# Kernel tuning notes

Hardware: AMD Instinct MI355X
Metric: run time of the kernel (lower is better)

## Reference

```python
import jax, jax.numpy as jnp
import numpy as np


def setup_inputs() -> dict:
    key = jax.random.key(0)
    k1, k2 = jax.random.split(key)
    x = jax.random.normal(k1, (16, 256, 4096), dtype=jnp.float32)          # [B, D, T]
    codebooks = jax.random.normal(k2, (8, 1024, 256), dtype=jnp.float32)   # [n_q, bins, D]
    return {"x": x, "codebooks": codebooks}


def _quantize_one(residual, embed):
    """residual: [B, T, D]; embed: [bins, D] -> (quantize [B,T,D], idx [B,T])."""
    # negative squared euclidean distance (encodec euclidean codebook)
    x_sq = jnp.sum(residual * residual, axis=-1, keepdims=True)            # [B, T, 1]
    e_sq = jnp.sum(embed * embed, axis=-1)                                  # [bins]
    dots = jnp.einsum("btd,nd->btn", residual, embed)                       # [B, T, bins]
    dist = -(x_sq - 2.0 * dots + e_sq)                                      # [B, T, bins]
    idx = jnp.argmax(dist, axis=-1)                                         # [B, T] int
    quantize = embed[idx]                                                   # gather [B, T, D]
    return quantize, idx


def reference(x, codebooks):
    """Residual VQ forward (inference path, EMA updates omitted).
    x: [B, D, T]; codebooks: [n_q, bins, D].
    Returns (quantized [B, D, T], codes [n_q, B, T]).
    """
    n_q = codebooks.shape[0]
    residual = jnp.transpose(x, (0, 2, 1))                                  # [B, T, D]
    quantized_out = jnp.zeros_like(residual)
    codes = []
    for q in range(n_q):  # small fixed structural loop over quantizer stages
        quantize, idx = _quantize_one(residual, codebooks[q])
        # straight-through estimator as in encodec VectorQuantization
        quantize = residual + jax.lax.stop_gradient(quantize - residual)
        residual = residual - quantize
        quantized_out = quantized_out + quantize
        codes.append(idx)
    quantized = jnp.transpose(quantized_out, (0, 2, 1))                     # [B, D, T]
    codes = jnp.stack(codes, axis=0)                                        # [n_q, B, T]
    return quantized, codes
```

## Files before the change

### kernel.cpp

```cpp
#include <hip/hip_runtime.h>


#define BB   16
#define DD   256
#define TT   4096
#define NQ   8
#define BINS 1024
#define DELTA 4.0f
#define SOFF  8192.0f
#define OUTQ ((size_t)BB * DD * TT)

typedef _Float16 half8 __attribute__((ext_vector_type(8)));
typedef float    facc  __attribute__((ext_vector_type(4)));

#define MFMA16(A, B, C) __builtin_amdgcn_mfma_f32_16x16x32_f16((A), (B), (C), 0, 0, 0)

__global__ __launch_bounds__(256)
void rvq_pack_h16(const float* __restrict__ cb, _Float16* __restrict__ pks) {
    int gid = blockIdx.x * 256 + threadIdx.x;
    int s   = gid & 7;
    int bin = (gid >> 3) & 1023;
    int q   = gid >> 13;
    const float* src = cb + ((size_t)(q * BINS + bin)) * DD + s * 32;
    int cc    = q * 32 + (bin >> 5);
    int nf    = (bin >> 4) & 1;
    int c     = bin & 15;
    int plane = nf * 8 + s;
    size_t base = (size_t)cc * 8192 + (size_t)plane * 512 + c * 8;
    #pragma unroll
    for (int g = 0; g < 4; ++g) {
        float4 v0 = *(const float4*)(src + g * 8);
        float4 v1 = *(const float4*)(src + g * 8 + 4);
        float vv[8] = { v0.x, v0.y, v0.z, v0.w, v1.x, v1.y, v1.z, v1.w };
        half8 h8;
        #pragma unroll
        for (int j = 0; j < 8; ++j) h8[j] = (_Float16)vv[j];
        *(half8*)&pks[base + g * 128] = h8;
    }
}

__global__ __launch_bounds__(256)
void rvq_esq_off(const float* __restrict__ cb, float* __restrict__ hoff) {
    int q = blockIdx.x;
    const float* e = cb + (size_t)q * BINS * DD;
    for (int bin = threadIdx.x; bin < BINS; bin += 256) {
        const float4* row = (const float4*)(e + (size_t)bin * DD);
        float s = 0.f;
        #pragma unroll 8
        for (int i = 0; i < DD / 4; ++i) {
            float4 v = row[i];
            s += v.x * v.x + v.y * v.y + v.z * v.z + v.w * v.w;
        }
        hoff[q * BINS + bin] = SOFF - 8.0f * s;
    }
}

__global__ __launch_bounds__(256, 2)
void rvq_mfma7_kernel(const float* __restrict__ x, const float* __restrict__ cb,
                      const _Float16* __restrict__ pks, const float* __restrict__ hoff,
                      float* __restrict__ out)
{
    __shared__ alignas(16) _Float16 btile[2][2][16][512];
    __shared__ float esq_lds[BINS];
    __shared__ unsigned short best_lds[4][32];
    __shared__ unsigned short hist_lds[4][NQ][32];

    const int tid = threadIdx.x;
    const int w   = tid >> 6;
    const int l   = tid & 63;
    const int c   = l & 15;
    const int g   = l >> 4;

    const int blk = blockIdx.x;
    const int b   = blk >> 5;
    const int t0  = (blk & 31) * 128;
    const int tw  = t0 + w * 32;

    const char* gsrc0 = (const char*)pks + w * 8192 + (l << 4);

    auto issue_pair = [&](int p, int bu) {
        p &= 127;
        const char* src = gsrc0 + (size_t)p * 32768;
        char* dst = (char*)(&btile[bu][0][0][0]) + w * 8192;
        #pragma unroll
        for (int i = 0; i < 8; ++i) {
            __builtin_amdgcn_global_load_lds(
                (const __attribute__((address_space(1))) unsigned int*)(src + i * 1024),
                (__attribute__((address_space(3))) unsigned int*)(dst + i * 1024),
                16, 0, 0);
        }
    };

    issue_pair(0, 0);

    half8 rh[2][8], rl[2][8];
    {
        const float* xb = x + (size_t)b * DD * TT;
        #pragma unroll
        for (int s = 0; s < 8; ++s) {
            #pragma unroll
            for (int j = 0; j < 8; ++j) {
                int d = s * 32 + g * 8 + j;
                #pragma unroll
                for (int m = 0; m < 2; ++m) {
                    int t = tw + m * 16 + c;
                    float v = 16.0f * xb[(size_t)d * TT + t];
                    _Float16 h = (_Float16)v;
                    rh[m][s][j] = h;
                    rl[m][s][j] = (_Float16)(v - (float)h);
                }
            }
        }
    }
    {
        float4 v = *(const float4*)(hoff + tid * 4);
        *(float4*)&esq_lds[tid * 4] = v;
    }
    __syncthreads();

    float p1[2][4], p2[2][4], p3[2][4];

    auto reset_slots = [&]() {
        #pragma unroll
        for (int m = 0; m < 2; ++m)
            #pragma unroll
            for (int j = 0; j < 4; ++j) { p1[m][j] = 0.f; p2[m][j] = 0.f; p3[m][j] = 0.f; }
    };

    auto compute_chunk = [&](int bu, int pc, int ch) {
        facc a00 = {0.f,0.f,0.f,0.f}, a01 = {0.f,0.f,0.f,0.f};
        facc a10 = {0.f,0.f,0.f,0.f}, a11 = {0.f,0.f,0.f,0.f};
        const int roff = g * 128 + c * 8;
        const float q0 = esq_lds[ch * 32 + c];
        const float q1 = esq_lds[ch * 32 + 16 + c];
        const _Float16 (*bt)[512] = btile[bu][pc];

        __builtin_amdgcn_s_setprio(1);
        #pragma unroll
        for (int s = 0; s < 8; ++s) {
            half8 b0 = *(const half8*)&bt[s][roff];
            half8 b1 = *(const half8*)&bt[8 + s][roff];
            a00 = MFMA16(rh[0][s], b0, a00);
            a10 = MFMA16(rh[1][s], b0, a10);
            a01 = MFMA16(rh[0][s], b1, a01);
            a11 = MFMA16(rh[1][s], b1, a11);
        }
        __builtin_amdgcn_s_setprio(0);

        const unsigned idx0 = 1023u - (unsigned)(ch * 32 + c);
        const unsigned idx1 = idx0 - 16u;
        #pragma unroll
        for (int fm = 0; fm < 2; ++fm) {
            #pragma unroll
            for (int fj = 0; fj < 4; ++fj) {
                float s0 = (fm ? a10[fj] : a00[fj]) + q0;
                float s1 = (fm ? a11[fj] : a01[fj]) + q1;
                float v0 = __builtin_bit_cast(float,
                             (__builtin_bit_cast(unsigned, s0) & ~1023u) | idx0);
                float v1 = __builtin_bit_cast(float,
                             (__builtin_bit_cast(unsigned, s1) & ~1023u) | idx1);
                float h1 = fmaxf(p1[fm][fj], v0), l1 = fminf(p1[fm][fj], v0);
                float h2 = fmaxf(p2[fm][fj], l1), l2 = fminf(p2[fm][fj], l1);
                p1[fm][fj] = h1; p2[fm][fj] = h2; p3[fm][fj] = fmaxf(p3[fm][fj], l2);
                h1 = fmaxf(p1[fm][fj], v1); l1 = fminf(p1[fm][fj], v1);
                h2 = fmaxf(p2[fm][fj], l1); l2 = fminf(p2[fm][fj], l1);
                p1[fm][fj] = h1; p2[fm][fj] = h2; p3[fm][fj] = fmaxf(p3[fm][fj], l2);
            }
        }
    };

    auto refine3 = [&](int tkl, int qq, int c1, int c2, int c3) -> int {
        int t = tw + tkl;
        double pa = 0.0, pb = 0.0, pc = 0.0;
        const float* e1p = cb + (size_t)(qq * BINS + c1) * DD;
        const float* e2p = cb + (size_t)(qq * BINS + c2) * DD;
        const float* e3p = cb + (size_t)(qq * BINS + c3) * DD;
        #pragma unroll
        for (int dd = 0; dd < 4; ++dd) {
            int d = l * 4 + dd;
            float rv = x[((size_t)b * DD + d) * TT + t];
            for (int k = 0; k < qq; ++k) {
                int hb = hist_lds[w][k][tkl];
                rv -= cb[(size_t)(k * BINS + hb) * DD + d];
            }
            float e1v = e1p[d], e2v = e2p[d], e3v = e3p[d];
            pa += (double)e1v * (2.0 * (double)rv - (double)e1v);
            pb += (double)e2v * (2.0 * (double)rv - (double)e2v);
            pc += (double)e3v * (2.0 * (double)rv - (double)e3v);
        }
        #pragma unroll
        for (int mk = 1; mk < 64; mk <<= 1) {
            pa += __shfl_xor(pa, mk);
            pb += __shfl_xor(pb, mk);
            pc += __shfl_xor(pc, mk);
        }
        int wbin = c1; double pw = pa;
        if (pb > pw || (pb == pw && c2 < wbin)) { pw = pb; wbin = c2; }
        if (pc > pw || (pc == pw && c3 < wbin)) { pw = pc; wbin = c3; }
        return wbin;
    };

    auto stage_end = [&](int qq) {
        int  bch[2][4], cn2[2][4], cn3[2][4];
        bool gate[2][4];
        #pragma unroll
        for (int fm = 0; fm < 2; ++fm) {
            #pragma unroll
            for (int fj = 0; fj < 4; ++fj) {
                float a1 = p1[fm][fj], a2 = p2[fm][fj], a3 = p3[fm][fj];
                #pragma unroll
                for (int mk = 1; mk < 16; mk <<= 1) {
                    float b1 = __shfl_xor(a1, mk);
                    float b2 = __shfl_xor(a2, mk);
                    float b3 = __shfl_xor(a3, mk);
                    float lo1 = fminf(a1, b1);
                    float m22 = fmaxf(a2, b2);
                    float r1  = fmaxf(a1, b1);
                    float r2  = fmaxf(lo1, m22);
                    float r3  = fmaxf(fminf(lo1, m22), fmaxf(fminf(a2, b2), fmaxf(a3, b3)));
                    a1 = r1; a2 = r2; a3 = r3;
                }
                bch[fm][fj] = 1023 - (int)(__builtin_bit_cast(unsigned, a1) & 1023u);
                cn2[fm][fj] = 1023 - (int)(__builtin_bit_cast(unsigned, a2) & 1023u);
                cn3[fm][fj] = 1023 - (int)(__builtin_bit_cast(unsigned, a3) & 1023u);
                gate[fm][fj] = (a1 - a2 <= DELTA);
            }
        }
        bool anyg = gate[0][0] | gate[0][1] | gate[0][2] | gate[0][3]
                  | gate[1][0] | gate[1][1] | gate[1][2] | gate[1][3];
        if (__any(anyg)) {
            #pragma unroll
            for (int fm = 0; fm < 2; ++fm) {
                #pragma unroll
                for (int fj = 0; fj < 4; ++fj) {
                    unsigned long long nm = __ballot(gate[fm][fj]);
                    if (nm) {
                        for (int g2 = 0; g2 < 4; ++g2) {
                            if ((nm >> (g2 * 16)) & 1ull) {
                                int c1 = __shfl(bch[fm][fj], g2 * 16);
                                int c2 = __shfl(cn2[fm][fj], g2 * 16);
                                int c3 = __shfl(cn3[fm][fj], g2 * 16);
                                int tkl = fm * 16 + g2 * 4 + fj;
                                int wb = refine3(tkl, qq, c1, c2, c3);
                                if (g == g2) bch[fm][fj] = wb;
                            }
                        }
                    }
                }
            }
        }

        if (c == 0) {
            #pragma unroll
            for (int fm = 0; fm < 2; ++fm)
                #pragma unroll
                for (int fj = 0; fj < 4; ++fj) {
                    int tkl = fm * 16 + g * 4 + fj;
                    best_lds[w][tkl] = (unsigned short)bch[fm][fj];
                    hist_lds[w][qq][tkl] = (unsigned short)bch[fm][fj];
                    out[OUTQ + ((size_t)qq * BB + b) * TT + tw + tkl] = (float)bch[fm][fj];
                }
        }

        #pragma unroll
        for (int m = 0; m < 2; ++m) {
            int bin = best_lds[w][m * 16 + c];
            const float* ep = cb + (size_t)(qq * BINS + bin) * DD + g * 8;
            #pragma unroll
            for (int s = 0; s < 8; ++s) {
                float4 e0 = *(const float4*)(ep + s * 32);
                float4 e1 = *(const float4*)(ep + s * 32 + 4);
                float ev[8] = { e0.x, e0.y, e0.z, e0.w, e1.x, e1.y, e1.z, e1.w };
                #pragma unroll
                for (int j = 0; j < 8; ++j) {
                    float rv = (float)rh[m][s][j] + (float)rl[m][s][j];
                    float nr = rv - 16.0f * ev[j];
                    _Float16 nh = (_Float16)nr;
                    rh[m][s][j] = nh;
                    rl[m][s][j] = (_Float16)(nr - (float)nh);
                }
            }
        }
    };

    int buf = 0;
    #pragma unroll 1
    for (int q = 0; q < NQ; ++q) {
        reset_slots();
        #pragma unroll 1
        for (int p = 0; p < 16; ++p) {
            issue_pair(q * 16 + p + 1, buf ^ 1);
            compute_chunk(buf, 0, 2 * p);
            compute_chunk(buf, 1, 2 * p + 1);
            if (p == 15) stage_end(q);
            __syncthreads();
            buf ^= 1;
        }
        if (q + 1 < NQ) {
            float4 v = *(const float4*)(hoff + (q + 1) * BINS + tid * 4);
            *(float4*)&esq_lds[tid * 4] = v;
            __syncthreads();
        }
    }

    {
        const float* xb = x + (size_t)b * DD * TT;
        float* ob = out + (size_t)b * DD * TT;
        #pragma unroll
        for (int s = 0; s < 8; ++s)
            #pragma unroll
            for (int j = 0; j < 8; ++j) {
                int d = s * 32 + g * 8 + j;
                #pragma unroll
                for (int m = 0; m < 2; ++m) {
                    int t = tw + m * 16 + c;
                    float rv = ((float)rh[m][s][j] + (float)rl[m][s][j]) * 0.0625f;
                    ob[(size_t)d * TT + t] = xb[(size_t)d * TT + t] - rv;
                }
            }
    }
}

#define TOK_PER_BLK 32
#define BIN_CHUNK   128
#define KC          32
#define EPAD        36
#define RPAD        260
#define FDELTA      0.0078125f

#define FUPD2(S, BIN, B1, I1, B2, I2)                                        \
    if ((S) > (B2) || ((S) == (B2) && (BIN) < (I2))) {                      \
        if ((S) > (B1) || ((S) == (B1) && (BIN) < (I1))) {                  \
            B2 = B1; I2 = I1; B1 = (S); I1 = (BIN);                         \
        } else { B2 = (S); I2 = (BIN); }                                    \
    }

__global__ __launch_bounds__(256, 2)
void rvq_esq_kernel(const float* __restrict__ cb, float* __restrict__ esq) {
    int q = blockIdx.x;
    const float* e = cb + (size_t)q * BINS * DD;
    for (int bin = threadIdx.x; bin < BINS; bin += 256) {
        const float4* row = (const float4*)(e + (size_t)bin * DD);
        float s = 0.f;
        #pragma unroll 8
        for (int i = 0; i < DD / 4; ++i) {
            float4 v = row[i];
            s += v.x * v.x + v.y * v.y + v.z * v.z + v.w * v.w;
        }
        esq[q * BINS + bin] = s;
    }
}

__global__ __launch_bounds__(256, 2)
void rvq_main_kernel(const float* __restrict__ x, const float* __restrict__ cb,
                     const float* __restrict__ esq, float* __restrict__ out) {
    __shared__ float r_lds[TOK_PER_BLK][RPAD];
    __shared__ float e_lds[BIN_CHUNK][EPAD];
    __shared__ float red_s[16][2][TOK_PER_BLK];
    __shared__ int   red_i[16][2][TOK_PER_BLK];
    __shared__ int   best_lds2[TOK_PER_BLK];

    const int tid = threadIdx.x;
    const int blk = blockIdx.x;
    const int b   = blk >> 7;
    const int t0  = (blk & 127) * TOK_PER_BLK;

    {
        const int tl = tid & 31;
        const int d0 = (tid >> 5) * 32;
        const float* xp = x + (size_t)b * DD * TT + t0 + tl;
        for (int dd = 0; dd < 32; ++dd) {
            int d = d0 + dd;
            r_lds[tl][d] = xp[(size_t)d * TT];
        }
    }
    __syncthreads();

    const int ty = tid >> 4;
    const int tx = tid & 15;

    for (int q = 0; q < NQ; ++q) {
        const float* eb = cb + (size_t)q * BINS * DD;
        const float* es = esq + q * BINS;
        float b1[2] = {-1e30f, -1e30f}, b2[2] = {-1e30f, -1e30f};
        int   i1[2] = {0x7fffffff, 0x7fffffff}, i2[2] = {0x7fffffff, 0x7fffffff};

        for (int cch = 0; cch < BINS / BIN_CHUNK; ++cch) {
            float acc[2][8];
            #pragma unroll
            for (int i = 0; i < 2; ++i)
                #pragma unroll
                for (int j = 0; j < 8; ++j) acc[i][j] = 0.f;

            for (int kc = 0; kc < DD / KC; ++kc) {
                __syncthreads();
                {
                    const int col  = tid & 7;
                    const int row0 = tid >> 3;
                    const float* src = eb + (size_t)(cch * BIN_CHUNK) * DD + kc * KC;
                    #pragma unroll
                    for (int rr = 0; rr < 4; ++rr) {
                        int row = row0 + rr * 32;
                        float4 v = *(const float4*)(src + (size_t)row * DD + col * 4);
                        *(float4*)&e_lds[row][col * 4] = v;
                    }
                }
                __syncthreads();
                #pragma unroll
                for (int k4 = 0; k4 < KC / 4; ++k4) {
                    float4 r0 = *(const float4*)&r_lds[tx][kc * KC + k4 * 4];
                    float4 r1 = *(const float4*)&r_lds[tx + 16][kc * KC + k4 * 4];
                    #pragma unroll
                    for (int bi = 0; bi < 8; ++bi) {
                        float4 e4 = *(const float4*)&e_lds[ty + 16 * bi][k4 * 4];
                        acc[0][bi] += r0.x * e4.x + r0.y * e4.y + r0.z * e4.z + r0.w * e4.w;
                        acc[1][bi] += r1.x * e4.x + r1.y * e4.y + r1.z * e4.z + r1.w * e4.w;
                    }
                }
            }
            #pragma unroll
            for (int bi = 0; bi < 8; ++bi) {
                int bin = cch * BIN_CHUNK + ty + 16 * bi;
                float half_esq = 0.5f * es[bin];
                float s0 = acc[0][bi] - half_esq;
                float s1v = acc[1][bi] - half_esq;
                FUPD2(s0, bin, b1[0], i1[0], b2[0], i2[0]);
                FUPD2(s1v, bin, b1[1], i1[1], b2[1], i2[1]);
            }
        }

        #pragma unroll
        for (int k = 0; k < 2; ++k) {
            red_s[ty][k][tx]      = k ? b2[0] : b1[0];
            red_i[ty][k][tx]      = k ? i2[0] : i1[0];
            red_s[ty][k][tx + 16] = k ? b2[1] : b1[1];
            red_i[ty][k][tx + 16] = k ? i2[1] : i1[1];
        }
        __syncthreads();

        if (tid < TOK_PER_BLK) {
            float g1 = -1e30f, g2 = -1e30f; int gi1 = 0x7fffffff, gi2 = 0x7fffffff;
            #pragma unroll
            for (int j = 0; j < 16; ++j) {
                #pragma unroll
                for (int k = 0; k < 2; ++k) {
                    float s = red_s[j][k][tid]; int ii = red_i[j][k][tid];
                    FUPD2(s, ii, g1, gi1, g2, gi2);
                }
            }
            int bif;
            if (g1 - g2 <= FDELTA) {
                const float* rrow = r_lds[tid];
                double sc[2]; int id2[2] = { gi1, gi2 };
                for (int cc2 = 0; cc2 < 2; ++cc2) {
                    const float* ep = eb + (size_t)id2[cc2] * DD;
                    double acc2 = 0.0;
                    #pragma unroll 4
                    for (int d = 0; d < DD; ++d) {
                        double ev = (double)ep[d];
                        acc2 += ev * (2.0 * (double)rrow[d] - ev);
                    }
                    sc[cc2] = acc2;
                }
                bif = (sc[0] > sc[1] || (sc[0] == sc[1] && id2[0] < id2[1])) ? id2[0] : id2[1];
            } else {
                bif = gi1;
            }
            best_lds2[tid] = bif;
            out[OUTQ + (size_t)q * (BB * TT) + (size_t)b * TT + t0 + tid] = (float)bif;
        }
        __syncthreads();

        {
            const int tok  = tid >> 3;
            const int part = tid & 7;
            const int bin  = best_lds2[tok];
            const float* ep = eb + (size_t)bin * DD + part * 32;
            float* rp = &r_lds[tok][part * 32];
            #pragma unroll
            for (int dd = 0; dd < 32; ++dd) rp[dd] -= ep[dd];
        }
        __syncthreads();
    }

    {
        const int tl = tid & 31;
        const int d0 = (tid >> 5) * 32;
        const float* xp = x + (size_t)b * DD * TT + t0 + tl;
        float*       op = out + (size_t)b * DD * TT + t0 + tl;
        for (int dd = 0; dd < 32; ++dd) {
            int d = d0 + dd;
            op[(size_t)d * TT] = xp[(size_t)d * TT] - r_lds[tl][d];
        }
    }
}

extern "C" void kernel_launch(void* const* d_in, const int* in_sizes, int n_in,
                              void* d_out, int out_size, void* d_ws, size_t ws_size,
                              hipStream_t stream) {
    const float* x  = (const float*)d_in[0];
    const float* cb = (const float*)d_in[1];
    float* out = (float*)d_out;

    const size_t PKS_BYTES = (size_t)NQ * BINS * DD * 2;
    const size_t NEED = PKS_BYTES + (size_t)NQ * BINS * 4;

    if (ws_size >= NEED) {
        _Float16* pks = (_Float16*)d_ws;
        float* hoff = (float*)((char*)d_ws + PKS_BYTES);
        rvq_pack_h16<<<(NQ * BINS * 8) / 256, 256, 0, stream>>>(cb, pks);
        rvq_esq_off<<<NQ, 256, 0, stream>>>(cb, hoff);
        rvq_mfma7_kernel<<<512, 256, 0, stream>>>(x, cb, pks, hoff, out);
    } else {
        float* esq = (float*)d_ws;
        rvq_esq_kernel<<<NQ, 256, 0, stream>>>(cb, esq);
        rvq_main_kernel<<<(BB * TT) / TOK_PER_BLK, 256, 0, stream>>>(x, cb, esq, out);
    }
}
```

Baseline: 627.2 us.

## Triple-buffer codebook chunks with fine-grained vmcnt waits and med3 top-3 update

```diff
diff --git a/kernel.cpp b/kernel.cpp
--- a/kernel.cpp
+++ b/kernel.cpp
@@ -56,11 +56,11 @@
 }
 
 __global__ __launch_bounds__(256, 2)
-void rvq_mfma7_kernel(const float* __restrict__ x, const float* __restrict__ cb,
-                      const _Float16* __restrict__ pks, const float* __restrict__ hoff,
-                      float* __restrict__ out)
+void rvq_mfma10_kernel(const float* __restrict__ x, const float* __restrict__ cb,
+                       const _Float16* __restrict__ pks, const float* __restrict__ hoff,
+                       float* __restrict__ out)
 {
-    __shared__ alignas(16) _Float16 btile[2][2][16][512];
+    __shared__ alignas(16) _Float16 btile[3][16][512];
     __shared__ float esq_lds[BINS];
     __shared__ unsigned short best_lds[4][32];
     __shared__ unsigned short hist_lds[4][NQ][32];
@@ -76,22 +76,19 @@
     const int t0  = (blk & 31) * 128;
     const int tw  = t0 + w * 32;
 
-    const char* gsrc0 = (const char*)pks + w * 8192 + (l << 4);
-
-    auto issue_pair = [&](int p, int bu) {
-        p &= 127;
-        const char* src = gsrc0 + (size_t)p * 32768;
-        char* dst = (char*)(&btile[bu][0][0][0]) + w * 8192;
-        #pragma unroll
-        for (int i = 0; i < 8; ++i) {
+    const char* gsrc0 = (const char*)pks + w * 4096 + (l << 4);
+
+    auto issue_chunk = [&](int k, int bu) {
+        const char* src = gsrc0 + (size_t)k * 16384;
+        char* dst = (char*)(&btile[bu][0][0]) + w * 4096;
+        #pragma unroll
+        for (int i = 0; i < 4; ++i) {
             __builtin_amdgcn_global_load_lds(
                 (const __attribute__((address_space(1))) unsigned int*)(src + i * 1024),
                 (__attribute__((address_space(3))) unsigned int*)(dst + i * 1024),
                 16, 0, 0);
         }
     };
-
-    issue_pair(0, 0);
 
     half8 rh[2][8], rl[2][8];
     {
@@ -127,13 +124,13 @@
             for (int j = 0; j < 4; ++j) { p1[m][j] = 0.f; p2[m][j] = 0.f; p3[m][j] = 0.f; }
     };
 
-    auto compute_chunk = [&](int bu, int pc, int ch) {
+    auto compute_chunk = [&](int bu, int ch) {
         facc a00 = {0.f,0.f,0.f,0.f}, a01 = {0.f,0.f,0.f,0.f};
         facc a10 = {0.f,0.f,0.f,0.f}, a11 = {0.f,0.f,0.f,0.f};
         const int roff = g * 128 + c * 8;
         const float q0 = esq_lds[ch * 32 + c];
         const float q1 = esq_lds[ch * 32 + 16 + c];
-        const _Float16 (*bt)[512] = btile[bu][pc];
+        const _Float16 (*bt)[512] = btile[bu];
 
         __builtin_amdgcn_s_setprio(1);
         #pragma unroll
@@ -159,12 +156,14 @@
                              (__builtin_bit_cast(unsigned, s0) & ~1023u) | idx0);
                 float v1 = __builtin_bit_cast(float,
                              (__builtin_bit_cast(unsigned, s1) & ~1023u) | idx1);
-                float h1 = fmaxf(p1[fm][fj], v0), l1 = fminf(p1[fm][fj], v0);
-                float h2 = fmaxf(p2[fm][fj], l1), l2 = fminf(p2[fm][fj], l1);
-                p1[fm][fj] = h1; p2[fm][fj] = h2; p3[fm][fj] = fmaxf(p3[fm][fj], l2);
-                h1 = fmaxf(p1[fm][fj], v1); l1 = fminf(p1[fm][fj], v1);
-                h2 = fmaxf(p2[fm][fj], l1); l2 = fminf(p2[fm][fj], l1);
-                p1[fm][fj] = h1; p2[fm][fj] = h2; p3[fm][fj] = fmaxf(p3[fm][fj], l2);
+                float o1 = p1[fm][fj], o2 = p2[fm][fj], o3 = p3[fm][fj];
+                p1[fm][fj] = fmaxf(o1, v0);
+                p2[fm][fj] = __builtin_amdgcn_fmed3f(v0, o1, o2);
+                p3[fm][fj] = __builtin_amdgcn_fmed3f(v0, o2, o3);
+                o1 = p1[fm][fj]; o2 = p2[fm][fj]; o3 = p3[fm][fj];
+                p1[fm][fj] = fmaxf(o1, v1);
+                p2[fm][fj] = __builtin_amdgcn_fmed3f(v1, o1, o2);
+                p3[fm][fj] = __builtin_amdgcn_fmed3f(v1, o2, o3);
             }
         }
     };
@@ -283,19 +282,27 @@
         }
     };
 
-    int buf = 0;
     #pragma unroll 1
     for (int q = 0; q < NQ; ++q) {
         reset_slots();
+        const int base = q * 32;
+        issue_chunk(base + 0, 0);
+        issue_chunk(base + 1, 1);
         #pragma unroll 1
-        for (int p = 0; p < 16; ++p) {
-            issue_pair(q * 16 + p + 1, buf ^ 1);
-            compute_chunk(buf, 0, 2 * p);
-            compute_chunk(buf, 1, 2 * p + 1);
-            if (p == 15) stage_end(q);
-            __syncthreads();
-            buf ^= 1;
-        }
+        for (int ch = 0; ch < 32; ++ch) {
+            __builtin_amdgcn_sched_barrier(0);
+            if (ch < 31) {
+                asm volatile("s_waitcnt vmcnt(4)" ::: "memory");
+            } else {
+                asm volatile("s_waitcnt vmcnt(0)" ::: "memory");
+            }
+            __builtin_amdgcn_s_barrier();
+            __builtin_amdgcn_sched_barrier(0);
+            if (ch + 2 < 32) issue_chunk(base + ch + 2, (ch + 2) % 3);
+            compute_chunk(ch % 3, ch);
+        }
+        stage_end(q);
+        __syncthreads();
         if (q + 1 < NQ) {
             float4 v = *(const float4*)(hoff + (q + 1) * BINS + tid * 4);
             *(float4*)&esq_lds[tid * 4] = v;
@@ -510,7 +517,7 @@
         float* hoff = (float*)((char*)d_ws + PKS_BYTES);
         rvq_pack_h16<<<(NQ * BINS * 8) / 256, 256, 0, stream>>>(cb, pks);
         rvq_esq_off<<<NQ, 256, 0, stream>>>(cb, hoff);
-        rvq_mfma7_kernel<<<512, 256, 0, stream>>>(x, cb, pks, hoff, out);
+        rvq_mfma10_kernel<<<512, 256, 0, stream>>>(x, cb, pks, hoff, out);
     } else {
         float* esq = (float*)d_ws;
         rvq_esq_kernel<<<NQ, 256, 0, stream>>>(cb, esq);
```

Measured after the change: 653.4 us. 4.2% more time.

## Load codebook fragments directly into registers instead of LDS double-buffering

Applied to the files above, without the earlier changes.

```diff
diff --git a/kernel.cpp b/kernel.cpp
--- a/kernel.cpp
+++ b/kernel.cpp
@@ -22,11 +22,9 @@
     int bin = (gid >> 3) & 1023;
     int q   = gid >> 13;
     const float* src = cb + ((size_t)(q * BINS + bin)) * DD + s * 32;
-    int cc    = q * 32 + (bin >> 5);
-    int nf    = (bin >> 4) & 1;
+    int cc    = q * 64 + (bin >> 4);
     int c     = bin & 15;
-    int plane = nf * 8 + s;
-    size_t base = (size_t)cc * 8192 + (size_t)plane * 512 + c * 8;
+    size_t base = (size_t)cc * 4096 + (size_t)s * 512 + c * 8;
     #pragma unroll
     for (int g = 0; g < 4; ++g) {
         float4 v0 = *(const float4*)(src + g * 8);
@@ -56,11 +54,10 @@
 }
 
 __global__ __launch_bounds__(256, 2)
-void rvq_mfma7_kernel(const float* __restrict__ x, const float* __restrict__ cb,
-                      const _Float16* __restrict__ pks, const float* __restrict__ hoff,
-                      float* __restrict__ out)
+void rvq_mfma11_kernel(const float* __restrict__ x, const float* __restrict__ cb,
+                       const _Float16* __restrict__ pks, const float* __restrict__ hoff,
+                       float* __restrict__ out)
 {
-    __shared__ alignas(16) _Float16 btile[2][2][16][512];
     __shared__ float esq_lds[BINS];
     __shared__ unsigned short best_lds[4][32];
     __shared__ unsigned short hist_lds[4][NQ][32];
@@ -76,22 +73,7 @@
     const int t0  = (blk & 31) * 128;
     const int tw  = t0 + w * 32;
 
-    const char* gsrc0 = (const char*)pks + w * 8192 + (l << 4);
-
-    auto issue_pair = [&](int p, int bu) {
-        p &= 127;
-        const char* src = gsrc0 + (size_t)p * 32768;
-        char* dst = (char*)(&btile[bu][0][0][0]) + w * 8192;
-        #pragma unroll
-        for (int i = 0; i < 8; ++i) {
-            __builtin_amdgcn_global_load_lds(
-                (const __attribute__((address_space(1))) unsigned int*)(src + i * 1024),
-                (__attribute__((address_space(3))) unsigned int*)(dst + i * 1024),
-                16, 0, 0);
-        }
-    };
-
-    issue_pair(0, 0);
+    const char* pkbase = (const char*)pks + ((l >> 4) * 256 + (l & 15) * 16);
 
     half8 rh[2][8], rl[2][8];
     {
@@ -120,54 +102,38 @@
 
     float p1[2][4], p2[2][4], p3[2][4];
 
-    auto reset_slots = [&]() {
-        #pragma unroll
-        for (int m = 0; m < 2; ++m)
-            #pragma unroll
-            for (int j = 0; j < 4; ++j) { p1[m][j] = 0.f; p2[m][j] = 0.f; p3[m][j] = 0.f; }
-    };
-
-    auto compute_chunk = [&](int bu, int pc, int ch) {
-        facc a00 = {0.f,0.f,0.f,0.f}, a01 = {0.f,0.f,0.f,0.f};
-        facc a10 = {0.f,0.f,0.f,0.f}, a11 = {0.f,0.f,0.f,0.f};
-        const int roff = g * 128 + c * 8;
-        const float q0 = esq_lds[ch * 32 + c];
-        const float q1 = esq_lds[ch * 32 + 16 + c];
-        const _Float16 (*bt)[512] = btile[bu][pc];
-
-        __builtin_amdgcn_s_setprio(1);
-        #pragma unroll
-        for (int s = 0; s < 8; ++s) {
-            half8 b0 = *(const half8*)&bt[s][roff];
-            half8 b1 = *(const half8*)&bt[8 + s][roff];
-            a00 = MFMA16(rh[0][s], b0, a00);
-            a10 = MFMA16(rh[1][s], b0, a10);
-            a01 = MFMA16(rh[0][s], b1, a01);
-            a11 = MFMA16(rh[1][s], b1, a11);
-        }
-        __builtin_amdgcn_s_setprio(0);
-
-        const unsigned idx0 = 1023u - (unsigned)(ch * 32 + c);
-        const unsigned idx1 = idx0 - 16u;
-        #pragma unroll
-        for (int fm = 0; fm < 2; ++fm) {
-            #pragma unroll
-            for (int fj = 0; fj < 4; ++fj) {
-                float s0 = (fm ? a10[fj] : a00[fj]) + q0;
-                float s1 = (fm ? a11[fj] : a01[fj]) + q1;
-                float v0 = __builtin_bit_cast(float,
-                             (__builtin_bit_cast(unsigned, s0) & ~1023u) | idx0);
-                float v1 = __builtin_bit_cast(float,
-                             (__builtin_bit_cast(unsigned, s1) & ~1023u) | idx1);
-                float h1 = fmaxf(p1[fm][fj], v0), l1 = fminf(p1[fm][fj], v0);
-                float h2 = fmaxf(p2[fm][fj], l1), l2 = fminf(p2[fm][fj], l1);
-                p1[fm][fj] = h1; p2[fm][fj] = h2; p3[fm][fj] = fmaxf(p3[fm][fj], l2);
-                h1 = fmaxf(p1[fm][fj], v1); l1 = fminf(p1[fm][fj], v1);
-                h2 = fmaxf(p2[fm][fj], l1); l2 = fminf(p2[fm][fj], l1);
-                p1[fm][fj] = h1; p2[fm][fj] = h2; p3[fm][fj] = fmaxf(p3[fm][fj], l2);
-            }
-        }
-    };
+    half8 Bx[8], By[8];
+
+#define LOADB(BSET, K) do {                                                  \
+    const char* _src = pkbase + (size_t)(K) * 8192;                          \
+    _Pragma("unroll")                                                        \
+    for (int _s = 0; _s < 8; ++_s)                                           \
+        BSET[_s] = *(const half8*)(_src + _s * 1024);                        \
+} while (0)
+
+#define COMPUTE(BSET, CH) do {                                               \
+    facc _a0 = {0.f,0.f,0.f,0.f}, _a1 = {0.f,0.f,0.f,0.f};                   \
+    _Pragma("unroll")                                                        \
+    for (int _s = 0; _s < 8; ++_s) {                                         \
+        _a0 = MFMA16(rh[0][_s], BSET[_s], _a0);                              \
+        _a1 = MFMA16(rh[1][_s], BSET[_s], _a1);                              \
+    }                                                                        \
+    const float _q0 = esq_lds[(CH) * 16 + c];                                \
+    const unsigned _idx0 = 1023u - (unsigned)((CH) * 16 + c);                \
+    _Pragma("unroll")                                                        \
+    for (int _fm = 0; _fm < 2; ++_fm) {                                      \
+        _Pragma("unroll")                                                    \
+        for (int _fj = 0; _fj < 4; ++_fj) {                                  \
+            float _sv = (_fm ? _a1[_fj] : _a0[_fj]) + _q0;                   \
+            float _v = __builtin_bit_cast(float,                            \
+                         (__builtin_bit_cast(unsigned, _sv) & ~1023u) | _idx0); \
+            float _o1 = p1[_fm][_fj], _o2 = p2[_fm][_fj], _o3 = p3[_fm][_fj]; \
+            p1[_fm][_fj] = fmaxf(_o1, _v);                                   \
+            p2[_fm][_fj] = __builtin_amdgcn_fmed3f(_v, _o1, _o2);            \
+            p3[_fm][_fj] = __builtin_amdgcn_fmed3f(_v, _o2, _o3);            \
+        }                                                                    \
+    }                                                                        \
+} while (0)
 
     auto refine3 = [&](int tkl, int qq, int c1, int c2, int c3) -> int {
         int t = tw + tkl;
@@ -283,24 +249,31 @@
         }
     };
 
-    int buf = 0;
     #pragma unroll 1
     for (int q = 0; q < NQ; ++q) {
-        reset_slots();
+        #pragma unroll
+        for (int fm = 0; fm < 2; ++fm)
+            #pragma unroll
+            for (int fj = 0; fj < 4; ++fj) {
+                p1[fm][fj] = 0.f; p2[fm][fj] = 0.f; p3[fm][fj] = 0.f;
+            }
+        const int base = q * 64;
+        LOADB(Bx, base + 0);
         #pragma unroll 1
-        for (int p = 0; p < 16; ++p) {
-            issue_pair(q * 16 + p + 1, buf ^ 1);
-            compute_chunk(buf, 0, 2 * p);
-            compute_chunk(buf, 1, 2 * p + 1);
-            if (p == 15) stage_end(q);
-            __syncthreads();
-            buf ^= 1;
-        }
+        for (int p = 0; p < 32; ++p) {
+            const int ch = 2 * p;
+            LOADB(By, base + ch + 1);
+            COMPUTE(Bx, ch);
+            if (p < 31) LOADB(Bx, base + ch + 2);
+            COMPUTE(By, ch + 1);
+        }
+        stage_end(q);
+        __syncthreads();
         if (q + 1 < NQ) {
             float4 v = *(const float4*)(hoff + (q + 1) * BINS + tid * 4);
             *(float4*)&esq_lds[tid * 4] = v;
-            __syncthreads();
-        }
+        }
+        __syncthreads();
     }
 
     {
@@ -510,7 +483,7 @@
         float* hoff = (float*)((char*)d_ws + PKS_BYTES);
         rvq_pack_h16<<<(NQ * BINS * 8) / 256, 256, 0, stream>>>(cb, pks);
         rvq_esq_off<<<NQ, 256, 0, stream>>>(cb, hoff);
-        rvq_mfma7_kernel<<<512, 256, 0, stream>>>(x, cb, pks, hoff, out);
+        rvq_mfma11_kernel<<<512, 256, 0, stream>>>(x, cb, pks, hoff, out);
     } else {
         float* esq = (float*)d_ws;
         rvq_esq_kernel<<<NQ, 256, 0, stream>>>(cb, esq);
```

Result: no change. 622.9 us (-0.7%).
